# Kernel tuning notes

Hardware: AMD Instinct MI355X
Metric: run time of the kernel (lower is better)

Reference implementation:

```python
import jax, jax.numpy as jnp
import numpy as np
from jax import lax

N, C, A, K, D = 2, 256, 3, 20, 256  # batch, channels, anchors, topk person cells, rn_fc_dim
BOX = 4
SIZES = [(80, 128), (40, 64), (20, 32), (10, 16)]
DN = ('NCHW', 'OIHW', 'NCHW')


def _conv(x, w, b):
    return lax.conv_general_dilated(x, w, (1, 1), 'SAME', dimension_numbers=DN) + b[None, :, None, None]


def setup_inputs() -> dict:
    key = jax.random.key(0)
    ks = iter(jax.random.split(key, 40))
    d = {}
    for i, (h, w) in enumerate(SIZES):
        d['feat%d' % i] = jax.random.normal(next(ks), (N, C, h, w), jnp.float32)
    def wfn(shape, s=0.05):
        return jax.random.normal(next(ks), shape, jnp.float32) * s
    d['pc1_w'] = wfn((C, C, 3, 3)); d['pc1_b'] = jnp.zeros((C,), jnp.float32)
    d['pc2_w'] = wfn((C, C, 3, 3)); d['pc2_b'] = jnp.zeros((C,), jnp.float32)
    d['oc1_w'] = wfn((C, C, 3, 3)); d['oc1_b'] = jnp.zeros((C,), jnp.float32)
    d['oc2_w'] = wfn((C, C, 3, 3)); d['oc2_b'] = jnp.zeros((C,), jnp.float32)
    # relation-net FCs: first takes concat(object, person) -> 2C in
    d['rn1_w'] = wfn((D, 2 * C)); d['rn1_b'] = jnp.zeros((D,), jnp.float32)
    d['rn2_w'] = wfn((D, D)); d['rn2_b'] = jnp.zeros((D,), jnp.float32)
    # heads
    d['pl_w'] = wfn((A, C, 1, 1), 0.01); d['pl_b'] = jnp.zeros((A,), jnp.float32)
    d['pd_w'] = wfn((A * BOX, C, 1, 1), 0.01); d['pd_b'] = jnp.zeros((A * BOX,), jnp.float32)
    d['ol_w'] = wfn((A, D), 0.01); d['ol_b'] = jnp.zeros((A,), jnp.float32)
    d['od_w'] = wfn((A * BOX, C, 1, 1), 0.01); d['od_b'] = jnp.zeros((A * BOX,), jnp.float32)
    return d


def _find_top_cells(hidden, logits, topk):
    hid_l, sc_l = [], []
    for h_map, lg in zip(hidden, logits):
        n, c, H, W = h_map.shape
        cell_scores = jnp.max(lg, axis=1).reshape(n, -1)          # (N, HW)
        ts, tc = lax.top_k(cell_scores, topk)                      # (N, K)
        hv = h_map.reshape(n, c, -1)                               # (N, C, HW)
        hid_l.append(jnp.take_along_axis(hv, tc[:, None, :], axis=2))  # (N, C, K)
        sc_l.append(ts)
    scores = jnp.concatenate(sc_l, axis=1)                         # (N, L*K)
    hid = jnp.concatenate(hid_l, axis=2)                           # (N, C, L*K)
    _, keep = lax.top_k(scores, topk)
    return jnp.take_along_axis(hid, keep[:, None, :], axis=2)      # (N, C, K)


def _forward(feats, pc1_w, pc1_b, pc2_w, pc2_b, oc1_w, oc1_b, oc2_w, oc2_b,
             rn1_w, rn1_b, rn2_w, rn2_b, pl_w, pl_b, pd_w, pd_b, ol_w, ol_b, od_w, od_b):
    # person branch
    p_hid, p_log, p_del = [], [], []
    for x in feats:
        x = jax.nn.relu(_conv(x, pc1_w, pc1_b))
        x = jax.nn.relu(_conv(x, pc2_w, pc2_b))
        p_hid.append(x)
        p_log.append(_conv(x, pl_w, pl_b))
        p_del.append(_conv(x, pd_w, pd_b))
    topk_person = _find_top_cells(p_hid, p_log, K)                 # (N, C, K)
    pf = topk_person.transpose(0, 2, 1)                            # (N, K, C)
    # object branch: fc1(concat(o, p)) == o @ Wo.T + p @ Wp.T + b (concat order: object first)
    Wo, Wp = rn1_w[:, :C], rn1_w[:, C:]
    p_proj = jnp.einsum('nkc,dc->nkd', pf, Wp) + rn1_b             # (N, K, D)
    o_log, o_del = [], []
    for x in feats:
        n, _, H, W = x.shape
        y = jax.nn.relu(_conv(x, oc1_w, oc1_b))
        y = jax.nn.relu(_conv(y, oc2_w, oc2_b))
        o_del.append(_conv(y, od_w, od_b))
        yf = y.reshape(n, C, H * W).transpose(0, 2, 1)             # (N, HW, C)
        o_proj = jnp.einsum('nsc,dc->nsd', yf, Wo)                 # (N, HW, D)
        h = jax.nn.relu(o_proj[:, :, None, :] + p_proj[:, None, :, :])  # (N, HW, K, D)
        h = h.sum(axis=2)                                          # (N, HW, D)
        h = jax.nn.relu(jnp.einsum('nsd,ed->nse', h, rn2_w) + rn2_b)
        ol = jnp.einsum('nsd,ad->nsa', h, ol_w) + ol_b             # (N, HW, A)
        o_log.append(ol.transpose(0, 2, 1).reshape(n, A, H, W))
    return tuple(p_log) + tuple(p_del) + tuple(o_log) + tuple(o_del)


def reference(feat0, feat1, feat2, feat3, pc1_w, pc1_b, pc2_w, pc2_b, oc1_w, oc1_b, oc2_w, oc2_b,
              rn1_w, rn1_b, rn2_w, rn2_b, pl_w, pl_b, pd_w, pd_b, ol_w, ol_b, od_w, od_b):
    return _forward([feat0, feat1, feat2, feat3], pc1_w, pc1_b, pc2_w, pc2_b, oc1_w, oc1_b,
                    oc2_w, oc2_b, rn1_w, rn1_b, rn2_w, rn2_b, pl_w, pl_b, pd_w, pd_b,
                    ol_w, ol_b, od_w, od_b)
```

## Files before the change

### kernel.cpp

```cpp
#include <hip/hip_runtime.h>
#include <cstdint>
#include <cstddef>

typedef __bf16 bf16x8 __attribute__((ext_vector_type(8)));
typedef float  f32x16 __attribute__((ext_vector_type(16)));

union U16 { bf16x8 v; uint4 q; };
union U8  { __bf16 h[4]; unsigned long long u; };

typedef __attribute__((address_space(1))) const unsigned char gas_t;
typedef __attribute__((address_space(3))) unsigned char las_t;
__device__ __forceinline__ void async16(const void* g, void* l) {
    __builtin_amdgcn_global_load_lds((gas_t*)g, (las_t*)l, 16, 0, 0);
}

__device__ __forceinline__ int lvl256(int bx) {
    return (bx < 40) ? 0 : (bx < 50) ? 1 : (bx < 53) ? 2 : 3;
}
__device__ __forceinline__ int tbase256(int lv) {
    return (lv == 0) ? 0 : (lv == 1) ? 40 : (lv == 2) ? 50 : 53;
}
__device__ __forceinline__ size_t loffE(int lv) {
    return (lv == 0) ? 0 : (lv == 1) ? 5242880 : (lv == 2) ? 6553600 : 6881280;
}
__device__ __forceinline__ size_t plog_off(int lv) {
    return (lv == 0) ? 0 : (lv == 1) ? 61440 : (lv == 2) ? 76800 : 80640;
}
__device__ __forceinline__ size_t pdel_off(int lv) {
    return (lv == 0) ? 81600 : (lv == 1) ? 327360 : (lv == 2) ? 388800 : 404160;
}
__device__ __forceinline__ size_t olog_off(int lv) {
    return (lv == 0) ? 408000 : (lv == 1) ? 469440 : (lv == 2) ? 484800 : 488640;
}
__device__ __forceinline__ size_t odel_off(int lv) {
    return (lv == 0) ? 489600 : (lv == 1) ? 735360 : (lv == 2) ? 796800 : 812160;
}
__device__ __forceinline__ int soff_l(int lv) {
    return (lv == 0) ? 0 : (lv == 1) ? 20480 : (lv == 2) ? 25600 : 26880;
}

__global__ __launch_bounds__(256) void prep_all_k(
    const float* f0, const float* f1, const float* f2, const float* f3,
    const float* pc1w, const float* pc2w, const float* oc1w, const float* oc2w,
    const float* __restrict__ rn1w, const float* __restrict__ rn2w,
    const float* __restrict__ olw,
    __bf16* __restrict__ wtap, float* __restrict__ WpT,
    __bf16* __restrict__ Wo16, __bf16* __restrict__ rn216,
    __bf16* __restrict__ olw32,
    unsigned* __restrict__ zrow32, __bf16* __restrict__ x16)
{
    __shared__ float f[2304];
    int bid = blockIdx.x, tid = threadIdx.x;
    if (bid < 1024) {
        int which = bid >> 8, co = bid & 255;
        const float* srcw = (which == 0) ? pc1w : (which == 1) ? pc2w
                          : (which == 2) ? oc1w : oc2w;
        const float* src = srcw + (size_t)co * 2304;
        for (int i = tid; i < 2304; i += 256) f[i] = src[i];
        __syncthreads();
        __bf16* dst = wtap + (size_t)which * 589824;
        int cg = co >> 6, co64 = co & 63;
        for (int u = tid; u < 288; u += 256) {
            int t = u >> 5, rest = u & 31, c16 = rest >> 1, hf = rest & 1;
            int ci0 = c16 * 16 + hf * 8;
            U16 v;
#pragma unroll
            for (int j = 0; j < 8; ++j) v.v[j] = (__bf16)f[(ci0 + j) * 9 + t];
            *(uint4*)&dst[(size_t)t * 65536 + c16 * 4096 + cg * 1024 + hf * 512 + co64 * 8] = v.q;
        }
    } else if (bid < 1280) {
        int d = bid - 1024, c = tid;
        WpT[c * 256 + d] = rn1w[(size_t)d * 512 + 256 + c];
        Wo16[((c >> 4) * 256 + d) * 16 + (c & 15)] = (__bf16)rn1w[(size_t)d * 512 + c];
        rn216[((c >> 4) * 256 + d) * 16 + (c & 15)] = (__bf16)rn2w[(size_t)d * 256 + c];
        if (d == 0) zrow32[c] = 0u;
    } else if (bid < 3008) {
        int u = bid - 1280;
        int bx = u >> 5, rr = u & 31, n = rr >> 4, ch = rr & 15;
        int lv = lvl256(bx);
        int HW = 10240 >> (2 * lv);
        int p = (bx - tbase256(lv)) * 256 + tid;
        if (p >= HW) return;
        const float* fp = (lv == 0) ? f0 : (lv == 1) ? f1 : (lv == 2) ? f2 : f3;
        const float* src = fp + (size_t)n * 256 * HW + (size_t)ch * 16 * HW + p;
        U16 a, b;
#pragma unroll
        for (int j = 0; j < 8; ++j) a.v[j] = (__bf16)src[(size_t)j * HW];
#pragma unroll
        for (int j = 0; j < 8; ++j) b.v[j] = (__bf16)src[(size_t)(8 + j) * HW];
        size_t o = loffE(lv) + (size_t)n * HW * 256 + (((size_t)ch * HW + p) << 4);
        *(uint4*)&x16[o] = a.q;
        *(uint4*)&x16[o + 8] = b.q;
    } else {
        int e16 = bid - 3008;
        for (int idx = tid; idx < 512; idx += 256) {
            int co = idx >> 4, j = idx & 15;
            float v = (co < 3) ? olw[co * 256 + e16 * 16 + j] : 0.f;
            olw32[e16 * 512 + co * 16 + j] = (__bf16)v;
        }
    }
}

__global__ __launch_bounds__(256) void conv3x3_v6(
    const __bf16* __restrict__ inA, const __bf16* __restrict__ inB,
    const __bf16* __restrict__ wtA, const __bf16* __restrict__ wtB,
    const float* __restrict__ bA, const float* __restrict__ bB,
    const __bf16* __restrict__ zrow,
    __bf16* __restrict__ outA, __bf16* __restrict__ outB, int mode)
{
    __shared__ __bf16 Asm[2][9216];

    const int id = blockIdx.x;
    const int r8 = id & 7, q = id >> 3;
    int by, br, n, tile;
    if (mode == 0) {
        by = q & 3; br = (q >> 2) & 1;
        int T = ((q >> 3) << 3) + r8; if (T >= 108) return;
        n = T & 1; tile = T >> 1;
    } else if (mode == 1) {
        by = q & 3;
        int T2 = ((q >> 2) << 3) + r8; if (T2 >= 216) return;
        br = T2 & 1; n = (T2 >> 1) & 1; tile = T2 >> 2;
    } else {
        by = q & 3; br = 0;
        int T = ((q >> 2) << 3) + r8; if (T >= 108) return;
        n = T & 1; tile = T >> 1;
    }

    const int tid = threadIdx.x;
    const __bf16* in16 = br ? inB : inA;
    const __bf16* wt = br ? wtB : wtA;
    const float* bias = br ? bB : bA;
    __bf16* outp = br ? outB : outA;

    const int lv = lvl256(tile);
    const int lg2W = 7 - lv;
    const int W = 1 << lg2W, H = 80 >> lv;
    const int HW = 10240 >> (2 * lv);
    const size_t ioff = loffE(lv) + (size_t)n * HW * 256;
    const __bf16* inb = in16 + ioff;

    const int sp0 = (tile - tbase256(lv)) << 8;
    const int npix = min(256, HW - sp0);

    const int w = tid >> 6, l64 = tid & 63;
    const int lane = l64 & 31, half = l64 >> 5;
    const int pix0 = (w << 6) + lane, pix1 = pix0 + 32;
    const int cobase = by << 6;

    int boff0[9], boff1[9];
    {
        const int y0 = sp0 >> lg2W;
        const int py0 = pix0 >> lg2W, px0 = pix0 & (W - 1);
        const int py1 = pix1 >> lg2W, px1 = pix1 & (W - 1);
#pragma unroll
        for (int dy = 0; dy < 3; ++dy)
#pragma unroll
            for (int dx = 0; dx < 3; ++dx) {
                int t = dy * 3 + dx;
                int gy0 = y0 + py0 + dy - 1, gx0 = px0 + dx - 1;
                boff0[t] = ((unsigned)gy0 < (unsigned)H && (unsigned)gx0 < (unsigned)W)
                           ? (((gy0 << lg2W) + gx0) * 32 + half * 16) : -1;
                int gy1 = y0 + py1 + dy - 1, gx1 = px1 + dx - 1;
                boff1[t] = ((unsigned)gy1 < (unsigned)H && (unsigned)gx1 < (unsigned)W)
                           ? (((gy1 << lg2W) + gx1) * 32 + half * 16) : -1;
            }
    }
    const __bf16* zp = zrow + (half << 3);

    const char* wtb = (const char*)wt + (by * 2048);
    auto stage = [&](int c16, int buf) {
        const char* base = wtb + (size_t)c16 * 8192;
        for (int u = w; u < 18; u += 4) {
            int t = u >> 1, hf = u & 1;
            async16(base + (size_t)t * 131072 + hf * 1024 + l64 * 16,
                    &Asm[buf][u * 512]);
        }
    };

    f32x16 acc00 = {}, acc01 = {}, acc10 = {}, acc11 = {};

    stage(0, 0);
    int buf = 0;
    for (int c16 = 0; c16 < 16; ++c16) {
        __syncthreads();
        if (c16 < 15) stage(c16 + 1, buf ^ 1);
        const char* curB = (const char*)inb + (size_t)c16 * HW * 32;
        const __bf16* Ab = &Asm[buf][0];
#pragma unroll
        for (int t = 0; t < 9; ++t) {
            bf16x8 a0 = *(const bf16x8*)&Ab[t * 1024 + half * 512 + lane * 8];
            bf16x8 a1 = *(const bf16x8*)&Ab[t * 1024 + half * 512 + 256 + lane * 8];
            const __bf16* q0 = (boff0[t] >= 0) ? (const __bf16*)(curB + boff0[t]) : zp;
            const __bf16* q1 = (boff1[t] >= 0) ? (const __bf16*)(curB + boff1[t]) : zp;
            bf16x8 b0 = *(const bf16x8*)q0;
            bf16x8 b1 = *(const bf16x8*)q1;
            acc00 = __builtin_amdgcn_mfma_f32_32x32x16_bf16(a0, b0, acc00, 0, 0, 0);
            acc01 = __builtin_amdgcn_mfma_f32_32x32x16_bf16(a0, b1, acc01, 0, 0, 0);
            acc10 = __builtin_amdgcn_mfma_f32_32x32x16_bf16(a1, b0, acc10, 0, 0, 0);
            acc11 = __builtin_amdgcn_mfma_f32_32x32x16_bf16(a1, b1, acc11, 0, 0, 0);
        }
        buf ^= 1;
    }
    const int pixg0 = sp0 + pix0, pixg1 = sp0 + pix1;
    const bool ok0 = (pix0 < npix), ok1 = (pix1 < npix);
#pragma unroll
    for (int b = 0; b < 2; ++b) {
        const f32x16& A0 = b ? acc10 : acc00;
        const f32x16& A1 = b ? acc11 : acc01;
#pragma unroll
        for (int qq = 0; qq < 4; ++qq) {
            int co0 = cobase + b * 32 + qq * 8 + half * 4;
            float4 bq = *(const float4*)&bias[co0];
            U8 v0, v1;
            v0.h[0] = (__bf16)fmaxf(A0[qq * 4 + 0] + bq.x, 0.f);
            v0.h[1] = (__bf16)fmaxf(A0[qq * 4 + 1] + bq.y, 0.f);
            v0.h[2] = (__bf16)fmaxf(A0[qq * 4 + 2] + bq.z, 0.f);
            v0.h[3] = (__bf16)fmaxf(A0[qq * 4 + 3] + bq.w, 0.f);
            v1.h[0] = (__bf16)fmaxf(A1[qq * 4 + 0] + bq.x, 0.f);
            v1.h[1] = (__bf16)fmaxf(A1[qq * 4 + 1] + bq.y, 0.f);
            v1.h[2] = (__bf16)fmaxf(A1[qq * 4 + 2] + bq.z, 0.f);
            v1.h[3] = (__bf16)fmaxf(A1[qq * 4 + 3] + bq.w, 0.f);
            size_t base = ioff + (((size_t)(co0 >> 4) * HW) << 4) + (co0 & 15);
            if (ok0) *(unsigned long long*)&outp[base + ((size_t)pixg0 << 4)] = v0.u;
            if (ok1) *(unsigned long long*)&outp[base + ((size_t)pixg1 << 4)] = v1.u;
        }
    }
}

__global__ __launch_bounds__(256) void heads_k(
    const __bf16* __restrict__ h16p, const __bf16* __restrict__ h16o,
    const float* __restrict__ plw, const float* __restrict__ plb,
    const float* __restrict__ pdw, const float* __restrict__ pdb,
    const float* __restrict__ odw, const float* __restrict__ odb,
    float* __restrict__ out, float* __restrict__ scores)
{
    int bx = blockIdx.x, n = blockIdx.y, br = blockIdx.z;
    int lv = lvl256(bx);
    int HW = 10240 >> (2 * lv);
    int p = (bx - tbase256(lv)) * 256 + threadIdx.x;
    if (p >= HW) return;
    size_t ioff = loffE(lv) + (size_t)n * HW * 256;
    if (br == 0) {
        float acc[15];
#pragma unroll
        for (int a = 0; a < 15; ++a) acc[a] = 0.f;
        for (int ch = 0; ch < 16; ++ch) {
            size_t base = ioff + (((size_t)ch * HW + p) << 4);
            bf16x8 v0 = *(const bf16x8*)&h16p[base];
            bf16x8 v1 = *(const bf16x8*)&h16p[base + 8];
#pragma unroll
            for (int j = 0; j < 16; ++j) {
                float vv = (j < 8) ? (float)v0[j] : (float)v1[j - 8];
                int c = ch * 16 + j;
#pragma unroll
                for (int a = 0; a < 3; ++a)  acc[a]     = fmaf(plw[a * 256 + c], vv, acc[a]);
#pragma unroll
                for (int a = 0; a < 12; ++a) acc[3 + a] = fmaf(pdw[a * 256 + c], vv, acc[3 + a]);
            }
        }
        float sc = -INFINITY;
#pragma unroll
        for (int a = 0; a < 3; ++a) {
            float lg = acc[a] + plb[a];
            out[plog_off(lv) + ((size_t)n * 3 + a) * HW + p] = lg;
            sc = fmaxf(sc, lg);
        }
        scores[soff_l(lv) + (size_t)n * HW + p] = sc;
#pragma unroll
        for (int a = 0; a < 12; ++a)
            out[pdel_off(lv) + ((size_t)n * 12 + a) * HW + p] = acc[3 + a] + pdb[a];
    } else {
        float acc[12];
#pragma unroll
        for (int a = 0; a < 12; ++a) acc[a] = 0.f;
        for (int ch = 0; ch < 16; ++ch) {
            size_t base = ioff + (((size_t)ch * HW + p) << 4);
            bf16x8 v0 = *(const bf16x8*)&h16o[base];
            bf16x8 v1 = *(const bf16x8*)&h16o[base + 8];
#pragma unroll
            for (int j = 0; j < 16; ++j) {
                float vv = (j < 8) ? (float)v0[j] : (float)v1[j - 8];
                int c = ch * 16 + j;
#pragma unroll
                for (int a = 0; a < 12; ++a) acc[a] = fmaf(odw[a * 256 + c], vv, acc[a]);
            }
        }
#pragma unroll
        for (int a = 0; a < 12; ++a)
            out[odel_off(lv) + ((size_t)n * 12 + a) * HW + p] = acc[a] + odb[a];
    }
}

__global__ __launch_bounds__(256) void topk_lvl_k(
    const float* __restrict__ scores, float* __restrict__ lv_sc,
    int* __restrict__ lv_ix)
{
    int l = blockIdx.x, n = blockIdx.y;
    int HW = 10240 >> (2 * l);
    const float* sp = scores + soff_l(l) + (size_t)n * HW;
    int tid = threadIdx.x;
    __shared__ float sc[10240];
    __shared__ float wv4[4];
    __shared__ int wi4[4];
    __shared__ int bcast;
    for (int i = tid; i < HW; i += 256) sc[i] = sp[i];
    __syncthreads();
    float bv = -INFINITY; int bi = 0x7fffffff;
    for (int i = tid; i < HW; i += 256)
        if (sc[i] > bv) { bv = sc[i]; bi = i; }
    const int w = tid >> 6, lane = tid & 63;
    for (int r = 0; r < 20; ++r) {
        float cv = bv; int ci = bi;
#pragma unroll
        for (int off = 32; off > 0; off >>= 1) {
            float ov = __shfl_xor(cv, off);
            int oi = __shfl_xor(ci, off);
            if (ov > cv || (ov == cv && oi < ci)) { cv = ov; ci = oi; }
        }
        if (lane == 0) { wv4[w] = cv; wi4[w] = ci; }
        __syncthreads();
        if (tid == 0) {
            float mv = wv4[0]; int mi = wi4[0];
#pragma unroll
            for (int j = 1; j < 4; ++j)
                if (wv4[j] > mv || (wv4[j] == mv && wi4[j] < mi)) { mv = wv4[j]; mi = wi4[j]; }
            bcast = mi;
            int idx = (n * 4 + l) * 20 + r;
            lv_sc[idx] = mv;
            lv_ix[idx] = mi;
        }
        __syncthreads();
        int mi = bcast;
        if ((mi & 255) == tid) {
            sc[mi] = -INFINITY;
            bv = -INFINITY; bi = 0x7fffffff;
            for (int i = tid; i < HW; i += 256)
                if (sc[i] > bv) { bv = sc[i]; bi = i; }
        }
    }
}

__global__ __launch_bounds__(256) void sel_pproj_k(
    const float* __restrict__ lv_sc, const int* __restrict__ lv_ix,
    const __bf16* __restrict__ h16p, const float* __restrict__ WpT,
    const float* __restrict__ rn1b, float* __restrict__ pp)
{
    int n = blockIdx.x, tid = threadIdx.x;
    __shared__ int selL[20], selC[20];
    __shared__ float pfL[5120];
    __shared__ float wv2[2];
    __shared__ int wi2[2];
    __shared__ int bcast;
    float bv = -INFINITY; int bi = 0x7fffffff;
    if (tid < 80) { bv = lv_sc[n * 80 + tid]; bi = tid; }
    const int w = tid >> 6, lane = tid & 63;
    for (int r = 0; r < 20; ++r) {
        float cv = bv; int ci = bi;
#pragma unroll
        for (int off = 32; off > 0; off >>= 1) {
            float ov = __shfl_xor(cv, off);
            int oi = __shfl_xor(ci, off);
            if (ov > cv || (ov == cv && oi < ci)) { cv = ov; ci = oi; }
        }
        if (lane == 0 && w < 2) { wv2[w] = cv; wi2[w] = ci; }
        __syncthreads();
        if (tid == 0) {
            float mv = wv2[0]; int mi = wi2[0];
            if (wv2[1] > mv || (wv2[1] == mv && wi2[1] < mi)) { mv = wv2[1]; mi = wi2[1]; }
            bcast = mi;
            selL[r] = mi / 20;
            selC[r] = lv_ix[n * 80 + mi];
        }
        __syncthreads();
        if (bcast == bi) bv = -INFINITY;
    }
    for (int t = tid; t < 5120; t += 256) {
        int k = t >> 8, c = t & 255;
        int l = selL[k], cell = selC[k];
        int HW = 10240 >> (2 * l);
        pfL[k * 256 + c] =
            (float)h16p[loffE(l) + (size_t)n * HW * 256 +
                        (((size_t)(c >> 4) * HW + cell) << 4) + (c & 15)];
    }
    __syncthreads();
    float acc[20];
    float bb = rn1b[tid];
#pragma unroll
    for (int k = 0; k < 20; ++k) acc[k] = bb;
    for (int c = 0; c < 256; ++c) {
        float wv = WpT[c * 256 + tid];
#pragma unroll
        for (int k = 0; k < 20; ++k) acc[k] = fmaf(pfL[k * 256 + c], wv, acc[k]);
    }
#pragma unroll
    for (int k = 0; k < 20; ++k)
        pp[(size_t)n * 5120 + k * 256 + tid] = acc[k];
}

__global__ __launch_bounds__(256) void orel_k(
    const __bf16* __restrict__ H16o, const __bf16* __restrict__ Wo16,
    const __bf16* __restrict__ rn216, const __bf16* __restrict__ olw32,
    const float* __restrict__ pp, const float* __restrict__ rn2b,
    const float* __restrict__ olb, float* __restrict__ out)
{
    __shared__ __bf16 hb[16 * 64 * 24];
    __shared__ __bf16 pp16[5120];
    __shared__ float red[768];
    const int tid = threadIdx.x;
    const int n = blockIdx.y;
    int bx = blockIdx.x;
    int lv = (bx < 160) ? 0 : (bx < 200) ? 1 : (bx < 210) ? 2 : 3;
    int tb = (lv == 0) ? 0 : (lv == 1) ? 160 : (lv == 2) ? 200 : 210;
    int HW = 10240 >> (2 * lv);
    size_t yoff = loffE(lv) + (size_t)n * HW * 256;
    int p0 = (bx - tb) << 6;
    int npix = min(64, HW - p0);

    {
        const float* ps = pp + (size_t)n * 5120;
        for (int i = tid; i < 1280; i += 256) {
            float4 f = *(const float4*)&ps[i * 4];
            U8 v;
            v.h[0] = (__bf16)f.x; v.h[1] = (__bf16)f.y;
            v.h[2] = (__bf16)f.z; v.h[3] = (__bf16)f.w;
            *(unsigned long long*)&pp16[i * 4] = v.u;
        }
    }
    __syncthreads();

    const int w = tid >> 6, l64 = tid & 63;
    const int lane = l64 & 31, half = l64 >> 5;
    const int dbase = w << 6;

    f32x16 acc00 = {}, acc01 = {}, acc10 = {}, acc11 = {};
    for (int c16 = 0; c16 < 16; ++c16) {
        bf16x8 a0 = *(const bf16x8*)&Wo16[(((c16 << 8) + dbase + lane) << 4) + (half << 3)];
        bf16x8 a1 = *(const bf16x8*)&Wo16[(((c16 << 8) + dbase + 32 + lane) << 4) + (half << 3)];
        bf16x8 b0 = *(const bf16x8*)&H16o[yoff + (((size_t)c16 * HW + p0 + lane) << 4) + (half << 3)];
        bf16x8 b1 = *(const bf16x8*)&H16o[yoff + (((size_t)c16 * HW + p0 + 32 + lane) << 4) + (half << 3)];
        acc00 = __builtin_amdgcn_mfma_f32_32x32x16_bf16(a0, b0, acc00, 0, 0, 0);
        acc01 = __builtin_amdgcn_mfma_f32_32x32x16_bf16(a0, b1, acc01, 0, 0, 0);
        acc10 = __builtin_amdgcn_mfma_f32_32x32x16_bf16(a1, b0, acc10, 0, 0, 0);
        acc11 = __builtin_amdgcn_mfma_f32_32x32x16_bf16(a1, b1, acc11, 0, 0, 0);
    }
#pragma unroll
    for (int b = 0; b < 2; ++b) {
        const f32x16& A0 = b ? acc10 : acc00;
        const f32x16& A1 = b ? acc11 : acc01;
#pragma unroll
        for (int q = 0; q < 4; ++q) {
            int d0 = dbase + b * 32 + q * 8 + half * 4;
            float h0[4] = {0.f, 0.f, 0.f, 0.f}, h1[4] = {0.f, 0.f, 0.f, 0.f};
            for (int k = 0; k < 20; ++k) {
                U8 pk;
                pk.u = *(const unsigned long long*)&pp16[k * 256 + d0];
#pragma unroll
                for (int j = 0; j < 4; ++j) {
                    float pkv = (float)pk.h[j];
                    h0[j] += fmaxf(A0[q * 4 + j] + pkv, 0.f);
                    h1[j] += fmaxf(A1[q * 4 + j] + pkv, 0.f);
                }
            }
            U8 v0, v1;
#pragma unroll
            for (int j = 0; j < 4; ++j) { v0.h[j] = (__bf16)h0[j]; v1.h[j] = (__bf16)h1[j]; }
            *(unsigned long long*)&hb[((d0 >> 4) * 64 + lane) * 24 + (d0 & 15)] = v0.u;
            *(unsigned long long*)&hb[((d0 >> 4) * 64 + 32 + lane) * 24 + (d0 & 15)] = v1.u;
        }
    }
    __syncthreads();
    f32x16 e00 = {}, e01 = {}, e10 = {}, e11 = {};
    for (int d16 = 0; d16 < 16; ++d16) {
        bf16x8 a0 = *(const bf16x8*)&rn216[(((d16 << 8) + dbase + lane) << 4) + (half << 3)];
        bf16x8 a1 = *(const bf16x8*)&rn216[(((d16 << 8) + dbase + 32 + lane) << 4) + (half << 3)];
        bf16x8 b0 = *(const bf16x8*)&hb[(d16 * 64 + lane) * 24 + (half << 3)];
        bf16x8 b1 = *(const bf16x8*)&hb[(d16 * 64 + 32 + lane) * 24 + (half << 3)];
        e00 = __builtin_amdgcn_mfma_f32_32x32x16_bf16(a0, b0, e00, 0, 0, 0);
        e01 = __builtin_amdgcn_mfma_f32_32x32x16_bf16(a0, b1, e01, 0, 0, 0);
        e10 = __builtin_amdgcn_mfma_f32_32x32x16_bf16(a1, b0, e10, 0, 0, 0);
        e11 = __builtin_amdgcn_mfma_f32_32x32x16_bf16(a1, b1, e11, 0, 0, 0);
    }
    __syncthreads();
#pragma unroll
    for (int b = 0; b < 2; ++b) {
        const f32x16& A0 = b ? e10 : e00;
        const f32x16& A1 = b ? e11 : e01;
#pragma unroll
        for (int q = 0; q < 4; ++q) {
            int e0 = dbase + b * 32 + q * 8 + half * 4;
            float4 bb = *(const float4*)&rn2b[e0];
            U8 v0, v1;
            v0.h[0] = (__bf16)fmaxf(A0[q * 4 + 0] + bb.x, 0.f);
            v0.h[1] = (__bf16)fmaxf(A0[q * 4 + 1] + bb.y, 0.f);
            v0.h[2] = (__bf16)fmaxf(A0[q * 4 + 2] + bb.z, 0.f);
            v0.h[3] = (__bf16)fmaxf(A0[q * 4 + 3] + bb.w, 0.f);
            v1.h[0] = (__bf16)fmaxf(A1[q * 4 + 0] + bb.x, 0.f);
            v1.h[1] = (__bf16)fmaxf(A1[q * 4 + 1] + bb.y, 0.f);
            v1.h[2] = (__bf16)fmaxf(A1[q * 4 + 2] + bb.z, 0.f);
            v1.h[3] = (__bf16)fmaxf(A1[q * 4 + 3] + bb.w, 0.f);
            *(unsigned long long*)&hb[((e0 >> 4) * 64 + lane) * 24 + (e0 & 15)] = v0.u;
            *(unsigned long long*)&hb[((e0 >> 4) * 64 + 32 + lane) * 24 + (e0 & 15)] = v1.u;
        }
    }
    __syncthreads();
    f32x16 ol0 = {}, ol1 = {};
#pragma unroll
    for (int j = 0; j < 4; ++j) {
        int e16 = w * 4 + j;
        bf16x8 a = *(const bf16x8*)&olw32[e16 * 512 + lane * 16 + (half << 3)];
        bf16x8 b0 = *(const bf16x8*)&hb[(e16 * 64 + lane) * 24 + (half << 3)];
        bf16x8 b1 = *(const bf16x8*)&hb[(e16 * 64 + 32 + lane) * 24 + (half << 3)];
        ol0 = __builtin_amdgcn_mfma_f32_32x32x16_bf16(a, b0, ol0, 0, 0, 0);
        ol1 = __builtin_amdgcn_mfma_f32_32x32x16_bf16(a, b1, ol1, 0, 0, 0);
    }
    if (half == 0) {
#pragma unroll
        for (int r = 0; r < 3; ++r) {
            red[(r * 64 + lane) * 4 + w] = ol0[r];
            red[(r * 64 + lane + 32) * 4 + w] = ol1[r];
        }
    }
    __syncthreads();
    if (tid < 192) {
        int a = tid >> 6, px = tid & 63;
        if (px < npix) {
            float4 p4 = *(const float4*)&red[(a * 64 + px) * 4];
            out[olog_off(lv) + ((size_t)n * 3 + a) * HW + p0 + px] =
                olb[a] + p4.x + p4.y + p4.z + p4.w;
        }
    }
}

extern "C" void kernel_launch(void* const* d_in, const int* in_sizes, int n_in,
                              void* d_out, int out_size, void* d_ws, size_t ws_size,
                              hipStream_t stream)
{
    const float* feat[4] = {(const float*)d_in[0], (const float*)d_in[1],
                            (const float*)d_in[2], (const float*)d_in[3]};
    const float* pc1w = (const float*)d_in[4];  const float* pc1b = (const float*)d_in[5];
    const float* pc2w = (const float*)d_in[6];  const float* pc2b = (const float*)d_in[7];
    const float* oc1w = (const float*)d_in[8];  const float* oc1b = (const float*)d_in[9];
    const float* oc2w = (const float*)d_in[10]; const float* oc2b = (const float*)d_in[11];
    const float* rn1w = (const float*)d_in[12]; const float* rn1b = (const float*)d_in[13];
    const float* rn2w = (const float*)d_in[14]; const float* rn2b = (const float*)d_in[15];
    const float* plw  = (const float*)d_in[16]; const float* plb  = (const float*)d_in[17];
    const float* pdw  = (const float*)d_in[18]; const float* pdb  = (const float*)d_in[19];
    const float* olw  = (const float*)d_in[20]; const float* olb  = (const float*)d_in[21];
    const float* odw  = (const float*)d_in[22]; const float* odb  = (const float*)d_in[23];

    float* ws = (float*)d_ws;
    __bf16* bufA = (__bf16*)(ws);
    __bf16* bufB = (__bf16*)(ws + 3481600);
    __bf16* bufC = (__bf16*)(ws + 6963200);
    __bf16* wtap = (__bf16*)(ws + 10444800);
    __bf16* wt_pc1 = wtap;
    __bf16* wt_pc2 = wtap + 589824;
    __bf16* wt_oc1 = wtap + 2 * 589824;
    __bf16* wt_oc2 = wtap + 3 * 589824;
    __bf16* Wo16  = (__bf16*)(ws + 11624448);
    __bf16* rn216 = (__bf16*)(ws + 11657216);
    float* WpT    = ws + 11689984;
    float* scores = ws + 11755520;
    float* lv_sc  = ws + 11783040;
    int*   lv_ix  = (int*)(ws + 11783200);
    __bf16* olw32 = (__bf16*)(ws + 11783360);
    float* pp     = ws + 11793280;
    __bf16* zrow  = (__bf16*)(ws + 11803520);
    __bf16* bufD  = (__bf16*)(ws + 11803904);
    float* out    = (float*)d_out;

    const bool merged = ws_size >= (size_t)(11803904 + 3481600) * 4;

    hipLaunchKernelGGL(prep_all_k, dim3(3024), dim3(256), 0, stream,
                       feat[0], feat[1], feat[2], feat[3],
                       pc1w, pc2w, oc1w, oc2w, rn1w, rn2w, olw,
                       wtap, WpT, Wo16, rn216, olw32, (unsigned*)zrow, bufA);

    hipLaunchKernelGGL(conv3x3_v6, dim3(896), dim3(256), 0, stream,
                       bufA, bufA, wt_pc1, wt_oc1, pc1b, oc1b, zrow,
                       bufB, bufC, 0);

    __bf16* h16o;
    if (merged) {
        hipLaunchKernelGGL(conv3x3_v6, dim3(864), dim3(256), 0, stream,
                           bufB, bufC, wt_pc2, wt_oc2, pc2b, oc2b, zrow,
                           bufA, bufD, 1);
        h16o = bufD;
    } else {
        hipLaunchKernelGGL(conv3x3_v6, dim3(448), dim3(256), 0, stream,
                           bufB, bufB, wt_pc2, wt_pc2, pc2b, pc2b, zrow,
                           bufA, bufA, 2);
        hipLaunchKernelGGL(conv3x3_v6, dim3(448), dim3(256), 0, stream,
                           bufC, bufC, wt_oc2, wt_oc2, oc2b, oc2b, zrow,
                           bufB, bufB, 2);
        h16o = bufB;
    }

    hipLaunchKernelGGL(heads_k, dim3(54, 2, 2), dim3(256), 0, stream,
                       bufA, h16o, plw, plb, pdw, pdb, odw, odb, out, scores);

    hipLaunchKernelGGL(topk_lvl_k, dim3(4, 2), dim3(256), 0, stream,
                       scores, lv_sc, lv_ix);
    hipLaunchKernelGGL(sel_pproj_k, dim3(2), dim3(256), 0, stream,
                       lv_sc, lv_ix, bufA, WpT, rn1b, pp);

    hipLaunchKernelGGL(orel_k, dim3(213, 2), dim3(256), 0, stream,
                       h16o, Wo16, rn216, olw32, pp, rn2b, olb, out);
}
```

Before: 510.4 us.

## Double conv3x3 pixel tile to 512 per block for weight reuse

The 3x3 conv kernel now has each block cover 512 pixels instead of 256. Each wave holds four 32-pixel subtiles and eight accumulators, so every weight fragment staged in LDS feeds twice as many MFMAs. Grid sizes are halved to match, and launch bounds ask for 2 blocks per CU. The aim is to cut redundant weight staging and LDS traffic per output, at the cost of more registers (36 offsets plus 8 accumulators), fewer blocks for the GPU to spread out, and some padded waste on the small levels.

Result: slower. 581.0 us (+13.8%).

```diff
diff --git a/kernel.cpp b/kernel.cpp
--- a/kernel.cpp
+++ b/kernel.cpp
@@ -101,7 +101,7 @@
     }
 }
 
-__global__ __launch_bounds__(256) void conv3x3_v6(
+__global__ __launch_bounds__(256, 2) void conv3x3_v7(
     const __bf16* __restrict__ inA, const __bf16* __restrict__ inB,
     const __bf16* __restrict__ wtA, const __bf16* __restrict__ wtB,
     const float* __restrict__ bA, const float* __restrict__ bB,
@@ -112,20 +112,19 @@
 
     const int id = blockIdx.x;
     const int r8 = id & 7, q = id >> 3;
-    int by, br, n, tile;
+    int cg, br, T;
     if (mode == 0) {
-        by = q & 3; br = (q >> 2) & 1;
-        int T = ((q >> 3) << 3) + r8; if (T >= 108) return;
-        n = T & 1; tile = T >> 1;
+        int s = q & 7; cg = s & 3; br = s >> 2;
+        T = ((q >> 3) << 3) + r8;
     } else if (mode == 1) {
-        by = q & 3;
-        int T2 = ((q >> 2) << 3) + r8; if (T2 >= 216) return;
-        br = T2 & 1; n = (T2 >> 1) & 1; tile = T2 >> 2;
+        cg = q & 3;
+        int T2 = ((q >> 2) << 3) + r8;
+        br = T2 & 1; T = T2 >> 1;
     } else {
-        by = q & 3; br = 0;
-        int T = ((q >> 2) << 3) + r8; if (T >= 108) return;
-        n = T & 1; tile = T >> 1;
-    }
+        cg = q & 3; br = 0;
+        T = ((q >> 2) << 3) + r8;
+    }
+    const int n = T & 1, tile = T >> 1;
 
     const int tid = threadIdx.x;
     const __bf16* in16 = br ? inB : inA;
@@ -133,42 +132,40 @@
     const float* bias = br ? bB : bA;
     __bf16* outp = br ? outB : outA;
 
-    const int lv = lvl256(tile);
+    const int lv = (tile < 20) ? 0 : (tile < 25) ? 1 : (tile < 27) ? 2 : 3;
+    const int tb = (lv == 0) ? 0 : (lv == 1) ? 20 : (lv == 2) ? 25 : 27;
     const int lg2W = 7 - lv;
     const int W = 1 << lg2W, H = 80 >> lv;
     const int HW = 10240 >> (2 * lv);
     const size_t ioff = loffE(lv) + (size_t)n * HW * 256;
     const __bf16* inb = in16 + ioff;
 
-    const int sp0 = (tile - tbase256(lv)) << 8;
-    const int npix = min(256, HW - sp0);
+    const int p0 = (tile - tb) << 9;
+    const int npix = min(512, HW - p0);
 
     const int w = tid >> 6, l64 = tid & 63;
     const int lane = l64 & 31, half = l64 >> 5;
-    const int pix0 = (w << 6) + lane, pix1 = pix0 + 32;
-    const int cobase = by << 6;
-
-    int boff0[9], boff1[9];
-    {
-        const int y0 = sp0 >> lg2W;
-        const int py0 = pix0 >> lg2W, px0 = pix0 & (W - 1);
-        const int py1 = pix1 >> lg2W, px1 = pix1 & (W - 1);
+    const int pxbase = p0 + (w << 7);
+    const int cobase = cg << 6;
+
+    int bo[36];
+#pragma unroll
+    for (int s = 0; s < 4; ++s) {
+        int pix = pxbase + (s << 5) + lane;
+        int py = pix >> lg2W, px = pix & (W - 1);
 #pragma unroll
         for (int dy = 0; dy < 3; ++dy)
 #pragma unroll
             for (int dx = 0; dx < 3; ++dx) {
-                int t = dy * 3 + dx;
-                int gy0 = y0 + py0 + dy - 1, gx0 = px0 + dx - 1;
-                boff0[t] = ((unsigned)gy0 < (unsigned)H && (unsigned)gx0 < (unsigned)W)
-                           ? (((gy0 << lg2W) + gx0) * 32 + half * 16) : -1;
-                int gy1 = y0 + py1 + dy - 1, gx1 = px1 + dx - 1;
-                boff1[t] = ((unsigned)gy1 < (unsigned)H && (unsigned)gx1 < (unsigned)W)
-                           ? (((gy1 << lg2W) + gx1) * 32 + half * 16) : -1;
+                int gy = py + dy - 1, gx = px + dx - 1;
+                bo[(dy * 3 + dx) * 4 + s] =
+                    ((unsigned)gy < (unsigned)H && (unsigned)gx < (unsigned)W)
+                    ? (((gy << lg2W) + gx) * 32 + half * 16) : -1;
             }
     }
     const __bf16* zp = zrow + (half << 3);
 
-    const char* wtb = (const char*)wt + (by * 2048);
+    const char* wtb = (const char*)wt + (cg * 2048);
     auto stage = [&](int c16, int buf) {
         const char* base = wtb + (size_t)c16 * 8192;
         for (int u = w; u < 18; u += 4) {
@@ -178,7 +175,7 @@
         }
     };
 
-    f32x16 acc00 = {}, acc01 = {}, acc10 = {}, acc11 = {};
+    f32x16 acc[2][4] = {};
 
     stage(0, 0);
     int buf = 0;
@@ -191,39 +188,41 @@
         for (int t = 0; t < 9; ++t) {
             bf16x8 a0 = *(const bf16x8*)&Ab[t * 1024 + half * 512 + lane * 8];
             bf16x8 a1 = *(const bf16x8*)&Ab[t * 1024 + half * 512 + 256 + lane * 8];
-            const __bf16* q0 = (boff0[t] >= 0) ? (const __bf16*)(curB + boff0[t]) : zp;
-            const __bf16* q1 = (boff1[t] >= 0) ? (const __bf16*)(curB + boff1[t]) : zp;
-            bf16x8 b0 = *(const bf16x8*)q0;
-            bf16x8 b1 = *(const bf16x8*)q1;
-            acc00 = __builtin_amdgcn_mfma_f32_32x32x16_bf16(a0, b0, acc00, 0, 0, 0);
-            acc01 = __builtin_amdgcn_mfma_f32_32x32x16_bf16(a0, b1, acc01, 0, 0, 0);
-            acc10 = __builtin_amdgcn_mfma_f32_32x32x16_bf16(a1, b0, acc10, 0, 0, 0);
-            acc11 = __builtin_amdgcn_mfma_f32_32x32x16_bf16(a1, b1, acc11, 0, 0, 0);
+            bf16x8 b[4];
+#pragma unroll
+            for (int s = 0; s < 4; ++s) {
+                int o = bo[t * 4 + s];
+                const __bf16* qp = (o >= 0) ? (const __bf16*)(curB + o) : zp;
+                b[s] = *(const bf16x8*)qp;
+            }
+#pragma unroll
+            for (int s = 0; s < 4; ++s) {
+                acc[0][s] = __builtin_amdgcn_mfma_f32_32x32x16_bf16(a0, b[s], acc[0][s], 0, 0, 0);
+                acc[1][s] = __builtin_amdgcn_mfma_f32_32x32x16_bf16(a1, b[s], acc[1][s], 0, 0, 0);
+            }
         }
         buf ^= 1;
     }
-    const int pixg0 = sp0 + pix0, pixg1 = sp0 + pix1;
-    const bool ok0 = (pix0 < npix), ok1 = (pix1 < npix);
-#pragma unroll
-    for (int b = 0; b < 2; ++b) {
-        const f32x16& A0 = b ? acc10 : acc00;
-        const f32x16& A1 = b ? acc11 : acc01;
-#pragma unroll
-        for (int qq = 0; qq < 4; ++qq) {
-            int co0 = cobase + b * 32 + qq * 8 + half * 4;
-            float4 bq = *(const float4*)&bias[co0];
-            U8 v0, v1;
-            v0.h[0] = (__bf16)fmaxf(A0[qq * 4 + 0] + bq.x, 0.f);
-            v0.h[1] = (__bf16)fmaxf(A0[qq * 4 + 1] + bq.y, 0.f);
-            v0.h[2] = (__bf16)fmaxf(A0[qq * 4 + 2] + bq.z, 0.f);
-            v0.h[3] = (__bf16)fmaxf(A0[qq * 4 + 3] + bq.w, 0.f);
-            v1.h[0] = (__bf16)fmaxf(A1[qq * 4 + 0] + bq.x, 0.f);
-            v1.h[1] = (__bf16)fmaxf(A1[qq * 4 + 1] + bq.y, 0.f);
-            v1.h[2] = (__bf16)fmaxf(A1[qq * 4 + 2] + bq.z, 0.f);
-            v1.h[3] = (__bf16)fmaxf(A1[qq * 4 + 3] + bq.w, 0.f);
-            size_t base = ioff + (((size_t)(co0 >> 4) * HW) << 4) + (co0 & 15);
-            if (ok0) *(unsigned long long*)&outp[base + ((size_t)pixg0 << 4)] = v0.u;
-            if (ok1) *(unsigned long long*)&outp[base + ((size_t)pixg1 << 4)] = v1.u;
+#pragma unroll
+    for (int s = 0; s < 4; ++s) {
+        const bool ok = ((w << 7) + (s << 5)) < npix;
+        if (!ok) continue;
+        const int pixg = pxbase + (s << 5) + lane;
+#pragma unroll
+        for (int f = 0; f < 2; ++f) {
+            const f32x16& A = acc[f][s];
+#pragma unroll
+            for (int qq = 0; qq < 4; ++qq) {
+                int co0 = cobase + f * 32 + qq * 8 + half * 4;
+                float4 bq = *(const float4*)&bias[co0];
+                U8 v;
+                v.h[0] = (__bf16)fmaxf(A[qq * 4 + 0] + bq.x, 0.f);
+                v.h[1] = (__bf16)fmaxf(A[qq * 4 + 1] + bq.y, 0.f);
+                v.h[2] = (__bf16)fmaxf(A[qq * 4 + 2] + bq.z, 0.f);
+                v.h[3] = (__bf16)fmaxf(A[qq * 4 + 3] + bq.w, 0.f);
+                size_t base = ioff + (((size_t)(co0 >> 4) * HW) << 4) + (co0 & 15);
+                *(unsigned long long*)&outp[base + ((size_t)pixg << 4)] = v.u;
+            }
         }
     }
 }
@@ -577,21 +576,21 @@
                        pc1w, pc2w, oc1w, oc2w, rn1w, rn2w, olw,
                        wtap, WpT, Wo16, rn216, olw32, (unsigned*)zrow, bufA);
 
-    hipLaunchKernelGGL(conv3x3_v6, dim3(896), dim3(256), 0, stream,
+    hipLaunchKernelGGL(conv3x3_v7, dim3(448), dim3(256), 0, stream,
                        bufA, bufA, wt_pc1, wt_oc1, pc1b, oc1b, zrow,
                        bufB, bufC, 0);
 
     __bf16* h16o;
     if (merged) {
-        hipLaunchKernelGGL(conv3x3_v6, dim3(864), dim3(256), 0, stream,
+        hipLaunchKernelGGL(conv3x3_v7, dim3(448), dim3(256), 0, stream,
                            bufB, bufC, wt_pc2, wt_oc2, pc2b, oc2b, zrow,
                            bufA, bufD, 1);
         h16o = bufD;
     } else {
-        hipLaunchKernelGGL(conv3x3_v6, dim3(448), dim3(256), 0, stream,
+        hipLaunchKernelGGL(conv3x3_v7, dim3(224), dim3(256), 0, stream,
                            bufB, bufB, wt_pc2, wt_pc2, pc2b, pc2b, zrow,
                            bufA, bufA, 2);
-        hipLaunchKernelGGL(conv3x3_v6, dim3(448), dim3(256), 0, stream,
+        hipLaunchKernelGGL(conv3x3_v7, dim3(224), dim3(256), 0, stream,
                            bufC, bufC, wt_oc2, wt_oc2, oc2b, oc2b, zrow,
                            bufB, bufB, 2);
         h16o = bufB;
```
